# Optimization experiments

Measured on AMD Instinct MI355X. Metric: run time of the kernel, lower is better.

## Reference

```python
import jax, jax.numpy as jnp
import numpy as np

B, T, S = 4, 1024, 1024
E, H, D, M = 768, 12, 64, 3072
SCALE = 1.0 / (D ** 0.5)
EPS = 1e-5


def setup_inputs() -> dict:
    key = jax.random.key(0)
    ks = jax.random.split(key, 20)
    s = 0.02

    def n(k, shp):
        return jax.random.normal(k, shp, jnp.float32) * s

    return {
        "target": jax.random.normal(ks[0], (B, T, E), jnp.float32),
        "memory": jax.random.normal(ks[1], (B, S, E), jnp.float32),
        # self-attention: per-head Q/K/V projections stacked over heads [H,E,D]
        "sa_wq": n(ks[2], (H, E, D)), "sa_bq": jnp.zeros((H, D), jnp.float32),
        "sa_wk": n(ks[3], (H, E, D)), "sa_bk": jnp.zeros((H, D), jnp.float32),
        "sa_wv": n(ks[4], (H, E, D)), "sa_bv": jnp.zeros((H, D), jnp.float32),
        "sa_wo": n(ks[5], (H * D, E)), "sa_bo": jnp.zeros((E,), jnp.float32),
        # cross-attention
        "ca_wq": n(ks[6], (H, E, D)), "ca_bq": jnp.zeros((H, D), jnp.float32),
        "ca_wk": n(ks[7], (H, E, D)), "ca_bk": jnp.zeros((H, D), jnp.float32),
        "ca_wv": n(ks[8], (H, E, D)), "ca_bv": jnp.zeros((H, D), jnp.float32),
        "ca_wo": n(ks[9], (H * D, E)), "ca_bo": jnp.zeros((E,), jnp.float32),
        # layernorms
        "ln1_g": jnp.ones((E,), jnp.float32), "ln1_b": jnp.zeros((E,), jnp.float32),
        "ln2_g": jnp.ones((E,), jnp.float32), "ln2_b": jnp.zeros((E,), jnp.float32),
        "ln3_g": jnp.ones((E,), jnp.float32), "ln3_b": jnp.zeros((E,), jnp.float32),
        # FFN
        "ffn_w1": n(ks[10], (E, M)), "ffn_b1": jnp.zeros((M,), jnp.float32),
        "ffn_w2": n(ks[11], (M, E)), "ffn_b2": jnp.zeros((E,), jnp.float32),
    }


def layernorm(x, g, b):
    mu = jnp.mean(x, axis=-1, keepdims=True)
    var = jnp.mean(jnp.square(x - mu), axis=-1, keepdims=True)
    return (x - mu) * jax.lax.rsqrt(var + EPS) * g + b


def mha(q_in, k_in, v_in, wq, bq, wk, bk, wv, bv, wo, bo, mask=None):
    # batched equivalent of the per-head looped projections
    Q = jnp.einsum('bse,hed->bhsd', q_in, wq) + bq[None, :, None, :]
    K = jnp.einsum('bte,hed->bhtd', k_in, wk) + bk[None, :, None, :]
    V = jnp.einsum('bte,hed->bhtd', v_in, wv) + bv[None, :, None, :]
    scores = jnp.einsum('bhsd,bhtd->bhst', Q, K) * SCALE
    if mask is not None:
        scores = jnp.where(mask, scores, -jnp.inf)
    w = jax.nn.softmax(scores, axis=-1)
    o = jnp.einsum('bhst,bhtd->bhsd', w, V)  # [B,H,Sq,D]
    o = o.transpose(0, 2, 1, 3).reshape(q_in.shape[0], q_in.shape[1], H * D)
    return o @ wo + bo


def reference(target, memory,
              sa_wq, sa_bq, sa_wk, sa_bk, sa_wv, sa_bv, sa_wo, sa_bo,
              ca_wq, ca_bq, ca_wk, ca_bk, ca_wv, ca_bv, ca_wo, ca_bo,
              ln1_g, ln1_b, ln2_g, ln2_b, ln3_g, ln3_b,
              ffn_w1, ffn_b1, ffn_w2, ffn_b2):
    Tq = target.shape[1]
    causal = jnp.tril(jnp.ones((Tq, Tq), bool))  # [T,T], broadcasts over B,H
    # pre-norm self-attention + residual
    x = layernorm(target, ln1_g, ln1_b)
    x = mha(x, x, x, sa_wq, sa_bq, sa_wk, sa_bk, sa_wv, sa_bv, sa_wo, sa_bo, causal) + target
    # pre-norm cross-attention + residual
    res = x
    y = layernorm(x, ln2_g, ln2_b)
    x = mha(y, memory, memory, ca_wq, ca_bq, ca_wk, ca_bk, ca_wv, ca_bv, ca_wo, ca_bo) + res
    # pre-norm FFN (Linear -> GELU -> Linear) + residual
    res = x
    y = layernorm(x, ln3_g, ln3_b)
    x = jax.nn.gelu(y @ ffn_w1 + ffn_b1) @ ffn_w2 + ffn_b2 + res
    return x
```

## Files before the change

kernel.cpp:

```cpp
#include <hip/hip_runtime.h>
#include <hip/hip_bf16.h>
#include <stdint.h>

#define BB 4
#define TT 1024
#define SS 1024
#define EE 768
#define HH 12
#define DDIM 64
#define MM 3072
#define NROWS 4096
#define SCALE2 0.18033688011112042f

typedef unsigned short u16;
using short8 = __attribute__((ext_vector_type(8))) short;
using f32x4  = __attribute__((ext_vector_type(4))) float;

__device__ inline f32x4 mfma16(short8 a, short8 b, f32x4 c) {
  return __builtin_amdgcn_mfma_f32_16x16x32_bf16(a, b, c, 0, 0, 0);
}

__device__ inline float b2f(u16 u) {
  union { uint32_t i; float f; } z; z.i = ((uint32_t)u) << 16; return z.f;
}
__device__ inline u16 f2b(float f) {
  __hip_bfloat16 h = __float2bfloat16(f);
  return *reinterpret_cast<u16*>(&h);
}
__device__ inline float loadf(const float* p) { return *p; }
__device__ inline float loadf(const u16* p) { return b2f(*p); }

__device__ inline float tanh_f(float x) {
  float e = exp2f(x * 2.885390081777927f);
  return 1.0f - 2.0f / (e + 1.0f);
}
__device__ inline float gelu_f(float x) {
  const float k0 = 0.7978845608028654f;
  const float k1 = 0.044715f;
  float t = tanh_f(k0 * (x + k1 * x * x * x));
  return 0.5f * x * (1.0f + t);
}

__device__ inline void gload16(const u16* g, u16* l) {
  __builtin_amdgcn_global_load_lds(
      (const __attribute__((address_space(1))) unsigned int*)g,
      (__attribute__((address_space(3))) unsigned int*)l, 16, 0, 0);
}

__global__ __launch_bounds__(256) void prep_k(
    const float* __restrict__ target, const float* __restrict__ ln1_g,
    const float* __restrict__ ln1_b, u16* __restrict__ lnb,
    const float* __restrict__ mem, u16* __restrict__ memB,
    const float* __restrict__ bq3, const float* __restrict__ bk3,
    const float* __restrict__ bv3, float* __restrict__ d3,
    const float* __restrict__ bk2, const float* __restrict__ bv2,
    float* __restrict__ d2,
    const float* __restrict__ sa_wq, const float* __restrict__ sa_wk,
    const float* __restrict__ sa_wv, u16* __restrict__ wqkvT_sa,
    const float* __restrict__ ca_wq, const float* __restrict__ ca_wk,
    const float* __restrict__ ca_wv, u16* __restrict__ wqkvT_ca,
    const float* __restrict__ sa_wo, const float* __restrict__ ca_wo,
    u16* __restrict__ woT,
    const float* __restrict__ ffn_w1, u16* __restrict__ w1T,
    const float* __restrict__ ffn_w2, u16* __restrict__ w2T) {
  __shared__ u16 tile[32][34];
  __shared__ float red[8];
  const int blk = blockIdx.x, t = threadIdx.x;
  if (blk < 4096) {
    const float* xr = target + (size_t)blk * EE;
    float v0 = xr[t], v1 = xr[t + 256], v2 = xr[t + 512];
    float s = v0 + v1 + v2;
#pragma unroll
    for (int m = 32; m >= 1; m >>= 1) s += __shfl_xor(s, m);
    int wv = t >> 6, ln = t & 63;
    if (ln == 0) red[wv] = s;
    __syncthreads();
    float mean = (red[0] + red[1] + red[2] + red[3]) * (1.0f / EE);
    float e0 = v0 - mean, e1 = v1 - mean, e2 = v2 - mean;
    float s2 = e0 * e0 + e1 * e1 + e2 * e2;
#pragma unroll
    for (int m = 32; m >= 1; m >>= 1) s2 += __shfl_xor(s2, m);
    if (ln == 0) red[4 + wv] = s2;
    __syncthreads();
    float var = (red[4] + red[5] + red[6] + red[7]) * (1.0f / EE);
    float rstd = rsqrtf(var + 1e-5f);
    u16* yr = lnb + (size_t)blk * EE;
    yr[t]       = f2b(e0 * rstd * ln1_g[t]       + ln1_b[t]);
    yr[t + 256] = f2b(e1 * rstd * ln1_g[t + 256] + ln1_b[t + 256]);
    yr[t + 512] = f2b(e2 * rstd * ln1_g[t + 512] + ln1_b[t + 512]);
  } else if (blk < 7168) {
    int i = ((blk - 4096) * 256 + t) * 4;
    float4 f = *(const float4*)(mem + i);
    u16 o[4] = {f2b(f.x), f2b(f.y), f2b(f.z), f2b(f.w)};
    *(uint64_t*)(memB + i) = *(const uint64_t*)o;
  } else if (blk < 7177) {
    int i = (blk - 7168) * 256 + t;
    if (i < 768) d3[i] = bq3[i];
    else if (i < 1536) d3[i] = bk3[i - 768];
    else d3[i] = bv3[i - 1536];
  } else if (blk < 7183) {
    int i = (blk - 7177) * 256 + t;
    if (i < 768) d2[i] = bk2[i];
    else d2[i] = bv2[i - 768];
  } else {
    const float* ip; u16* op; int R, C, bx, by;
    int r = blk - 7183;
    if (r < 1728) {
      int u = r / 48, rr = r % 48; bx = rr & 1; by = rr >> 1;
      const float* s = (u < 12) ? sa_wq : (u < 24) ? sa_wk : sa_wv;
      ip = s + (size_t)(u % 12) * EE * DDIM;
      op = wqkvT_sa + (size_t)u * EE * DDIM;
      R = EE; C = DDIM;
    } else if (r < 3456) {
      r -= 1728;
      int u = r / 48, rr = r % 48; bx = rr & 1; by = rr >> 1;
      const float* s = (u < 12) ? ca_wq : (u < 24) ? ca_wk : ca_wv;
      ip = s + (size_t)(u % 12) * EE * DDIM;
      op = wqkvT_ca + (size_t)u * EE * DDIM;
      R = EE; C = DDIM;
    } else if (r < 4608) {
      r -= 3456;
      int u = r / 576, rr = r % 576; bx = rr % 24; by = rr / 24;
      ip = (u == 0) ? sa_wo : ca_wo;
      op = woT + (size_t)u * EE * EE;
      R = EE; C = EE;
    } else if (r < 6912) {
      r -= 4608; bx = r % 96; by = r / 96;
      ip = ffn_w1; op = w1T; R = EE; C = MM;
    } else {
      r -= 6912; bx = r % 24; by = r / 24;
      ip = ffn_w2; op = w2T; R = MM; C = EE;
    }
    int r0 = by * 32, c0 = bx * 32;
    int tx = t & 31, ty = t >> 5;
#pragma unroll
    for (int j = 0; j < 32; j += 8)
      tile[ty + j][tx] = f2b(ip[(size_t)(r0 + ty + j) * C + (c0 + tx)]);
    __syncthreads();
#pragma unroll
    for (int j = 0; j < 32; j += 8)
      op[(size_t)(c0 + ty + j) * R + (r0 + tx)] = tile[tx][ty + j];
  }
}

template <typename T>
__global__ __launch_bounds__(256) void layernorm_k(const T* __restrict__ x,
    const float* __restrict__ g, const float* __restrict__ b,
    u16* __restrict__ y) {
  int row = blockIdx.x, t = threadIdx.x;
  const T* xr = x + (size_t)row * EE;
  float v0 = loadf(xr + t), v1 = loadf(xr + t + 256), v2 = loadf(xr + t + 512);
  float s = v0 + v1 + v2;
#pragma unroll
  for (int m = 32; m >= 1; m >>= 1) s += __shfl_xor(s, m);
  __shared__ float red[8];
  int wv = t >> 6, ln = t & 63;
  if (ln == 0) red[wv] = s;
  __syncthreads();
  float mean = (red[0] + red[1] + red[2] + red[3]) * (1.0f / EE);
  float d0 = v0 - mean, d1 = v1 - mean, d2 = v2 - mean;
  float s2 = d0 * d0 + d1 * d1 + d2 * d2;
#pragma unroll
  for (int m = 32; m >= 1; m >>= 1) s2 += __shfl_xor(s2, m);
  if (ln == 0) red[4 + wv] = s2;
  __syncthreads();
  float var = (red[4] + red[5] + red[6] + red[7]) * (1.0f / EE);
  float rstd = rsqrtf(var + 1e-5f);
  u16* yr = y + (size_t)row * EE;
  yr[t]       = f2b(d0 * rstd * g[t]       + b[t]);
  yr[t + 256] = f2b(d1 * rstd * g[t + 256] + b[t + 256]);
  yr[t + 512] = f2b(d2 * rstd * g[t + 512] + b[t + 512]);
}

template <int RESMODE, bool GELU, int XCDSWZ, typename OutT>
__global__ __launch_bounds__(256) void gemm128_k(
    const u16* __restrict__ A, const u16* __restrict__ Bt,
    const float* __restrict__ bias, const void* __restrict__ res,
    OutT* __restrict__ C, int M, int N, int K) {
  __shared__ u16 As[2][128 * 32];
  __shared__ u16 Bs[2][128 * 32];
  int bx = blockIdx.x, by = blockIdx.y;
  if (XCDSWZ == 1) {
    const int nbx = N >> 7;
    int id = bx + nbx * by;
    int per = (nbx * (M >> 7)) >> 3;
    int sid = (id & 7) * per + (id >> 3);
    bx = sid % nbx; by = sid / nbx;
  } else if (XCDSWZ == 2) {
    const int nbx = N >> 7, hx = nbx >> 1, qy = (M >> 7) >> 2;
    int id = bx + nbx * by;
    int xcd = id & 7, j = id >> 3;
    int rx = xcd & 1, ry = xcd >> 1;
    bx = rx * hx + j % hx;
    by = ry * qy + j / hx;
  }
  const int bm = by * 128, bn = bx * 128;
  const int t = threadIdx.x;
  const int wave = t >> 6, lane = t & 63;
  const int wr = wave >> 1, wc = wave & 1;
  const int g = lane >> 4, li = lane & 15;
  f32x4 acc[4][4] = {};
  const size_t rowskip = (size_t)64 * K;
  const int scol = (((t & 3) ^ ((t >> 3) & 3)) * 8);
  const u16* Ag = A + (size_t)(bm + (t >> 2)) * K + scol;
  const u16* Bg = Bt + (size_t)(bn + (t >> 2)) * K + scol;

  gload16(Ag, &As[0][t * 8]);
  gload16(Ag + rowskip, &As[0][2048 + t * 8]);
  gload16(Bg, &Bs[0][t * 8]);
  gload16(Bg + rowskip, &Bs[0][2048 + t * 8]);
  __syncthreads();

  const int nsteps = K >> 5;
#define STEP128(CUR, NXT, SB)                                                  \
  {                                                                            \
    if ((SB) + 1 < nsteps) {                                                   \
      const int k0 = ((SB) + 1) << 5;                                          \
      gload16(Ag + k0, &As[NXT][t * 8]);                                       \
      gload16(Ag + rowskip + k0, &As[NXT][2048 + t * 8]);                      \
      gload16(Bg + k0, &Bs[NXT][t * 8]);                                       \
      gload16(Bg + rowskip + k0, &Bs[NXT][2048 + t * 8]);                      \
    }                                                                          \
    short8 af[4], bf[4];                                                       \
    _Pragma("unroll")                                                          \
    for (int i = 0; i < 4; i++) {                                              \
      const int ar = wr * 64 + i * 16 + li;                                    \
      af[i] = *(const short8*)(&As[CUR][ar * 32 + ((g ^ ((ar >> 1) & 3)) * 8)]); \
      const int br = wc * 64 + i * 16 + li;                                    \
      bf[i] = *(const short8*)(&Bs[CUR][br * 32 + ((g ^ ((br >> 1) & 3)) * 8)]); \
    }                                                                          \
    _Pragma("unroll")                                                          \
    for (int mi = 0; mi < 4; mi++)                                             \
      _Pragma("unroll")                                                        \
      for (int nj = 0; nj < 4; nj++)                                           \
        acc[mi][nj] = mfma16(af[mi], bf[nj], acc[mi][nj]);                     \
    __syncthreads();                                                           \
  }
  for (int s = 0; s < nsteps; s += 2) {
    STEP128(0, 1, s)
    STEP128(1, 0, s + 1)
  }
#undef STEP128

#pragma unroll
  for (int mi = 0; mi < 4; mi++)
#pragma unroll
    for (int nj = 0; nj < 4; nj++) {
      int n = bn + wc * 64 + nj * 16 + li;
      float bv = bias[n];
#pragma unroll
      for (int i = 0; i < 4; i++) {
        int m = bm + wr * 64 + mi * 16 + g * 4 + i;
        float val = acc[mi][nj][i] + bv;
        if (GELU) val = gelu_f(val);
        if (RESMODE == 1) val += ((const float*)res)[(size_t)m * N + n];
        else if (RESMODE == 2) val += b2f(((const u16*)res)[(size_t)m * N + n]);
        if constexpr (sizeof(OutT) == 2) C[(size_t)m * N + n] = f2b(val);
        else                             C[(size_t)m * N + n] = val;
      }
    }
}

__global__ __launch_bounds__(256) void gemm128_dual_k(
    const u16* __restrict__ A0, const u16* __restrict__ B0,
    const float* __restrict__ bias0, u16* __restrict__ C0, int N0, int nbx0,
    const u16* __restrict__ A1, const u16* __restrict__ B1,
    const float* __restrict__ bias1, u16* __restrict__ C1, int N1,
    u16* __restrict__ vtsa, u16* __restrict__ vtca,
    int M, int K) {
  __shared__ u16 As[2][128 * 64];
  __shared__ u16 Bs[2][128 * 64];
  const int id = blockIdx.x + 30 * blockIdx.y;
  const int xcd = id & 7, j = id >> 3;
  const int rx = xcd & 1, ry = xcd >> 1;
  int x, y;
  if (j < 72) { x = rx * 9 + j % 9;               y = ry * 8 + j / 9; }
  else        { int jj = j - 72; x = 18 + rx * 6 + jj % 6; y = ry * 8 + jj / 6; }
  const bool p1 = (x >= nbx0);
  const u16* A = p1 ? A1 : A0;
  const u16* Bt = p1 ? B1 : B0;
  const float* bias = p1 ? bias1 : bias0;
  u16* C = p1 ? C1 : C0;
  const int N = p1 ? N1 : N0;
  const int bn = (p1 ? x - nbx0 : x) * 128;
  const int bm = y * 128;
  const int t = threadIdx.x;
  const int wave = t >> 6, lane = t & 63;
  const int wr = wave >> 1, wc = wave & 1;
  const int g = lane >> 4, li = lane & 15;
  f32x4 acc[4][4] = {};
  const int srow = t >> 3;
  const int scolz = ((t & 7) * 8) ^ ((srow & 7) << 3);
  const size_t skip32 = (size_t)32 * K;
  const u16* Ag = A + (size_t)(bm + srow) * K + scolz;
  const u16* Bg = Bt + (size_t)(bn + srow) * K + scolz;

#pragma unroll
  for (int jj = 0; jj < 4; jj++) {
    gload16(Ag + jj * skip32, &As[0][jj * 2048 + t * 8]);
    gload16(Bg + jj * skip32, &Bs[0][jj * 2048 + t * 8]);
  }
  __syncthreads();

  const int nsteps = K >> 6;
#define STEPD(CUR, NXT, SB)                                                    \
  {                                                                            \
    if ((SB) + 1 < nsteps) {                                                   \
      const int k0 = ((SB) + 1) << 6;                                          \
      _Pragma("unroll")                                                        \
      for (int jj = 0; jj < 4; jj++) {                                         \
        gload16(Ag + jj * skip32 + k0, &As[NXT][jj * 2048 + t * 8]);           \
        gload16(Bg + jj * skip32 + k0, &Bs[NXT][jj * 2048 + t * 8]);           \
      }                                                                        \
    }                                                                          \
    _Pragma("unroll")                                                          \
    for (int kk = 0; kk < 2; kk++) {                                           \
      short8 af[4], bf[4];                                                     \
      _Pragma("unroll")                                                        \
      for (int i = 0; i < 4; i++) {                                            \
        const int ar = wr * 64 + i * 16 + li;                                  \
        af[i] = *(const short8*)(&As[CUR][ar * 64 + ((kk * 32 + g * 8) ^ ((ar & 7) << 3))]); \
        const int br = wc * 64 + i * 16 + li;                                  \
        bf[i] = *(const short8*)(&Bs[CUR][br * 64 + ((kk * 32 + g * 8) ^ ((br & 7) << 3))]); \
      }                                                                        \
      _Pragma("unroll")                                                        \
      for (int mi = 0; mi < 4; mi++)                                           \
        _Pragma("unroll")                                                      \
        for (int nj = 0; nj < 4; nj++)                                         \
          acc[mi][nj] = mfma16(af[mi], bf[nj], acc[mi][nj]);                   \
    }                                                                          \
    __syncthreads();                                                           \
  }
  for (int s = 0; s < nsteps; s += 2) {
    STEPD(0, 1, s)
    STEPD(1, 0, s + 1)
  }
#undef STEPD

  const int vbase = p1 ? 768 : 1536;
  if (bn < vbase) {
#pragma unroll
    for (int mi = 0; mi < 4; mi++)
#pragma unroll
      for (int nj = 0; nj < 4; nj++) {
        int n = bn + wc * 64 + nj * 16 + li;
        float bv = bias[n];
#pragma unroll
        for (int i = 0; i < 4; i++) {
          int m = bm + wr * 64 + mi * 16 + g * 4 + i;
          C[(size_t)m * N + n] = f2b(acc[mi][nj][i] + bv);
        }
      }
  } else {
    u16* vtX = p1 ? vtca : vtsa;
    u16* tl = &As[0][0];
    const int bb = bm >> 10;
    const int t0b = bm & 1023;
#pragma unroll
    for (int nj = 0; nj < 4; nj++) {
      __syncthreads();
      {
        int n = bn + wc * 64 + nj * 16 + li;
        float bv = bias[n];
#pragma unroll
        for (int mi = 0; mi < 4; mi++)
#pragma unroll
          for (int i = 0; i < 4; i++) {
            int ml = wr * 64 + mi * 16 + g * 4 + i;
            tl[(wc * 16 + li) * 132 + ml] = f2b(acc[mi][nj][i] + bv);
          }
      }
      __syncthreads();
      int lr = t >> 3, m0 = (t & 7) * 16;
      int n = bn + (lr >> 4) * 64 + nj * 16 + (lr & 15);
      int hd = n - vbase;
      uint4 v0 = *(uint4*)&tl[lr * 132 + m0];
      uint4 v1 = *(uint4*)&tl[lr * 132 + m0 + 8];
      u16* dst = vtX + (((size_t)(bb * HH + (hd >> 6))) << 16) +
                 ((size_t)(hd & 63) << 10) + t0b + m0;
      *(uint4*)dst = v0;
      *(uint4*)(dst + 8) = v1;
    }
  }
}

template <int RESMODE, bool GELU, bool XCDSWZ, typename OutT>
__global__ __launch_bounds__(256) void gemm64_k(
    const u16* __restrict__ A, const u16* __restrict__ Bt,
    const float* __restrict__ bias, const void* __restrict__ res,
    OutT* __restrict__ C, int M, int N, int K) {
  __shared__ u16 As[2][64 * 64];
  __shared__ u16 Bs[2][64 * 64];
  int bx = blockIdx.x, by = blockIdx.y;
  if (XCDSWZ) {
    const int nbx = N >> 6;
    int id = bx + nbx * by;
    int per = (nbx * (M >> 6)) >> 3;
    int sid = (id & 7) * per + (id >> 3);
    bx = sid % nbx; by = sid / nbx;
  }
  const int bm = by * 64, bn = bx * 64;
  const int t = threadIdx.x;
  const int wave = t >> 6, lane = t & 63;
  const int wr = wave >> 1, wc = wave & 1;
  const int g = lane >> 4, li = lane & 15;
  f32x4 acc[2][2] = {};
  const int srow = t >> 3;
  const int scolz = ((t & 7) * 8) ^ ((srow & 7) << 3);
  const size_t skip32 = (size_t)32 * K;
  const u16* Ag = A + (size_t)(bm + srow) * K + scolz;
  const u16* Bg = Bt + (size_t)(bn + srow) * K + scolz;

  gload16(Ag, &As[0][t * 8]);
  gload16(Ag + skip32, &As[0][2048 + t * 8]);
  gload16(Bg, &Bs[0][t * 8]);
  gload16(Bg + skip32, &Bs[0][2048 + t * 8]);
  __syncthreads();

  const int nsteps = K >> 6;
#define STEP64(CUR, NXT, SB)                                                   \
  {                                                                            \
    if ((SB) + 1 < nsteps) {                                                   \
      const int k0 = ((SB) + 1) << 6;                                          \
      gload16(Ag + k0, &As[NXT][t * 8]);                                       \
      gload16(Ag + skip32 + k0, &As[NXT][2048 + t * 8]);                       \
      gload16(Bg + k0, &Bs[NXT][t * 8]);                                       \
      gload16(Bg + skip32 + k0, &Bs[NXT][2048 + t * 8]);                       \
    }                                                                          \
    short8 af[2][2], bf[2][2];                                                 \
    _Pragma("unroll")                                                          \
    for (int mt = 0; mt < 2; mt++)                                             \
      _Pragma("unroll")                                                        \
      for (int kk = 0; kk < 2; kk++) {                                         \
        int ar = wr * 32 + mt * 16 + li;                                       \
        af[mt][kk] = *(const short8*)(&As[CUR][ar * 64 + ((kk * 32 + g * 8) ^ ((ar & 7) << 3))]); \
        int br = wc * 32 + mt * 16 + li;                                       \
        bf[mt][kk] = *(const short8*)(&Bs[CUR][br * 64 + ((kk * 32 + g * 8) ^ ((br & 7) << 3))]); \
      }                                                                        \
    _Pragma("unroll")                                                          \
    for (int mt = 0; mt < 2; mt++)                                             \
      _Pragma("unroll")                                                        \
      for (int nt = 0; nt < 2; nt++)                                           \
        _Pragma("unroll")                                                      \
        for (int kk = 0; kk < 2; kk++)                                         \
          acc[mt][nt] = mfma16(af[mt][kk], bf[nt][kk], acc[mt][nt]);           \
    __syncthreads();                                                           \
  }
  for (int s = 0; s < nsteps; s += 2) {
    STEP64(0, 1, s)
    STEP64(1, 0, s + 1)
  }
#undef STEP64

#pragma unroll
  for (int mt = 0; mt < 2; mt++)
#pragma unroll
    for (int nt = 0; nt < 2; nt++) {
      int n = bn + wc * 32 + nt * 16 + li;
      float bv = bias[n];
#pragma unroll
      for (int i = 0; i < 4; i++) {
        int m = bm + wr * 32 + mt * 16 + g * 4 + i;
        float val = acc[mt][nt][i] + bv;
        if (GELU) val = gelu_f(val);
        if (RESMODE == 1) val += ((const float*)res)[(size_t)m * N + n];
        else if (RESMODE == 2) val += b2f(((const u16*)res)[(size_t)m * N + n]);
        if constexpr (sizeof(OutT) == 2) C[(size_t)m * N + n] = f2b(val);
        else                             C[(size_t)m * N + n] = val;
      }
    }
}

template <bool CAUSAL>
__global__ __launch_bounds__(256) void attn4_k(
    const u16* __restrict__ Q, const u16* __restrict__ K,
    const u16* __restrict__ VT, u16* __restrict__ O,
    int ldq, int ldk) {
  int b, h, q0;
  if (CAUSAL) {
    int id = blockIdx.x;
    int cu = id & 255, slot = id >> 8;
    int q, hb;
    if (cu < 96) {
      int p = cu & 1, r = cu >> 1;
      q = (slot == 0 ? 0 : slot == 1 ? 6 : 14) + p;
      hb = r;
    } else if (cu < 192) {
      int c2 = cu - 96; int p = c2 & 1, r = c2 >> 1;
      q = (slot == 0 ? 2 : slot == 1 ? 8 : 12) + p;
      hb = r;
    } else if (cu < 224) {
      int c2 = cu - 192;
      int p = c2 & 1, r = c2 >> 1;
      if (slot == 0)      { q = 10;    hb = c2; }
      else if (slot == 1) { q = 11;    hb = c2; }
      else                { q = 4 + p; hb = r; }
    } else {
      int c2 = cu - 224;
      int p = c2 & 1, r = c2 >> 1;
      if (slot == 0)      { q = 4;      hb = 16 + c2; }
      else if (slot == 1) { q = 5;      hb = 16 + c2; }
      else                { q = 10 + p; hb = 32 + r; }
    }
    h = hb % HH; b = hb / HH; q0 = q * 64;
  } else {
    int id = blockIdx.x + 16 * (blockIdx.y + HH * (int)blockIdx.z);
    int sid = (id & 7) * 96 + (id >> 3);
    q0 = (sid & 15) * 64;
    int yz = sid >> 4;
    h = yz % HH; b = yz / HH;
  }
  int tid = threadIdx.x, wave = tid >> 6, lane = tid & 63;
  int g = lane >> 4, li = lane & 15;
  const u16* Qb = Q + (size_t)b * TT * ldq + h * DDIM;
  const u16* Kb = K + (size_t)b * SS * ldk + h * DDIM;
  const u16* Vb = VT + (size_t)(b * HH + h) * DDIM * SS;
  u16* Ob = O + (size_t)b * TT * EE + h * DDIM;

  __shared__ u16 Ks[128 * 64];
  __shared__ u16 Vs[64 * 128];
  u16* Psw = &Ks[wave * 2048];

  int qrow = q0 + wave * 16 + li;
  short8 qf0 = *(const short8*)(Qb + (size_t)qrow * ldq + g * 8);
  short8 qf1 = *(const short8*)(Qb + (size_t)qrow * ldq + 32 + g * 8);

  f32x4 accO[4] = {};
  float lrow[4] = {0.f, 0.f, 0.f, 0.f};

  const int krow = tid >> 3;
  const int vrow = tid >> 4;
  const int qmax = q0 + wave * 16 + 15;

  int kvEnd = CAUSAL ? (((q0 + 64 + 127) >> 7) << 7) : SS;
  for (int kv0 = 0; kv0 < kvEnd; kv0 += 128) {
#pragma unroll
    for (int j = 0; j < 4; j++) {
      int kr = j * 32 + krow;
      int kc = ((tid & 7) * 8) ^ ((kr & 7) << 3);
      gload16(Kb + (size_t)(kv0 + kr) * ldk + kc, &Ks[j * 2048 + tid * 8]);
    }
#pragma unroll
    for (int j = 0; j < 4; j++) {
      int vr = j * 16 + vrow;
      int vc = ((tid & 15) * 8) ^ ((vr & 15) << 3);
      gload16(Vb + (size_t)vr * SS + kv0 + vc, &Vs[j * 2048 + tid * 8]);
    }
    __syncthreads();

    {
      const bool needMask = CAUSAL && (kv0 + 127 > qmax);
      f32x4 s[8];
#pragma unroll
      for (int kt = 0; kt < 8; kt++) {
        int kr = kt * 16 + li;
        int sw = (kr & 7) << 3;
        short8 kf0 = *(const short8*)(&Ks[kr * 64 + ((g * 8) ^ sw)]);
        short8 kf1 = *(const short8*)(&Ks[kr * 64 + ((g * 8 + 32) ^ sw)]);
        f32x4 z = {};
        z = mfma16(qf0, kf0, z);
        z = mfma16(qf1, kf1, z);
        s[kt] = z;
      }
      __syncthreads();

      float rsum[4] = {0.f, 0.f, 0.f, 0.f};
#pragma unroll
      for (int kt = 0; kt < 8; kt++)
#pragma unroll
        for (int i = 0; i < 4; i++) {
          float sv = s[kt][i] * SCALE2;
          if (needMask) {
            int qi = q0 + wave * 16 + g * 4 + i;
            int ti = kv0 + kt * 16 + li;
            if (ti > qi) sv = -1e30f;
          }
          float p = exp2f(sv);
          s[kt][i] = p;
          rsum[i] += p;
        }
#pragma unroll
      for (int msk = 1; msk < 16; msk <<= 1)
#pragma unroll
        for (int i = 0; i < 4; i++) rsum[i] += __shfl_xor(rsum[i], msk);
#pragma unroll
      for (int i = 0; i < 4; i++) lrow[i] += rsum[i];

#pragma unroll
      for (int kt = 0; kt < 8; kt++)
#pragma unroll
        for (int i = 0; i < 4; i++) {
          int row = g * 4 + i;
          Psw[row * 128 + ((kt * 16 + li) ^ ((row & 15) << 3))] = f2b(s[kt][i]);
        }

#pragma unroll
      for (int tc = 0; tc < 4; tc++) {
        short8 pf = *(const short8*)(&Psw[li * 128 + ((tc * 32 + g * 8) ^ ((li & 15) << 3))]);
#pragma unroll
        for (int dt = 0; dt < 4; dt++) {
          int vr = dt * 16 + li;
          short8 vf = *(const short8*)(&Vs[vr * 128 + ((tc * 32 + g * 8) ^ ((vr & 15) << 3))]);
          accO[dt] = mfma16(pf, vf, accO[dt]);
        }
      }
    }
    __syncthreads();
  }

#pragma unroll
  for (int i = 0; i < 4; i++) {
    float inv = 1.0f / lrow[i];
    int q = q0 + wave * 16 + g * 4 + i;
#pragma unroll
    for (int dt = 0; dt < 4; dt++)
      Ob[(size_t)q * EE + dt * 16 + li] = f2b(accO[dt][i] * inv);
  }
}

static inline void* wsoff(void* ws, size_t& off, size_t bytes) {
  void* p = (char*)ws + off;
  off += (bytes + 255) & ~(size_t)255;
  return p;
}

extern "C" void kernel_launch(void* const* d_in, const int* in_sizes, int n_in,
                              void* d_out, int out_size, void* d_ws, size_t ws_size,
                              hipStream_t stream) {
  const float* target = (const float*)d_in[0];
  const float* memory = (const float*)d_in[1];
  const float* sa_wq = (const float*)d_in[2];  const float* sa_bq = (const float*)d_in[3];
  const float* sa_wk = (const float*)d_in[4];  const float* sa_bk = (const float*)d_in[5];
  const float* sa_wv = (const float*)d_in[6];  const float* sa_bv = (const float*)d_in[7];
  const float* sa_wo = (const float*)d_in[8];  const float* sa_bo = (const float*)d_in[9];
  const float* ca_wq = (const float*)d_in[10]; const float* ca_bq = (const float*)d_in[11];
  const float* ca_wk = (const float*)d_in[12]; const float* ca_bk = (const float*)d_in[13];
  const float* ca_wv = (const float*)d_in[14]; const float* ca_bv = (const float*)d_in[15];
  const float* ca_wo = (const float*)d_in[16]; const float* ca_bo = (const float*)d_in[17];
  const float* ln1_g = (const float*)d_in[18]; const float* ln1_b = (const float*)d_in[19];
  const float* ln2_g = (const float*)d_in[20]; const float* ln2_b = (const float*)d_in[21];
  const float* ln3_g = (const float*)d_in[22]; const float* ln3_b = (const float*)d_in[23];
  const float* ffn_w1 = (const float*)d_in[24]; const float* ffn_b1 = (const float*)d_in[25];
  const float* ffn_w2 = (const float*)d_in[26]; const float* ffn_b2 = (const float*)d_in[27];

  size_t off = 0;
  const size_t WB = (size_t)EE * EE * 2;
  u16* wqkvT_sa = (u16*)wsoff(d_ws, off, 3 * WB);
  u16* wqT_ca   = (u16*)wsoff(d_ws, off, WB);
  u16* wkvT_ca  = (u16*)wsoff(d_ws, off, 2 * WB);
  u16* woT_sa   = (u16*)wsoff(d_ws, off, WB);
  u16* woT_ca   = (u16*)wsoff(d_ws, off, WB);
  u16* w1T      = (u16*)wsoff(d_ws, off, (size_t)EE * MM * 2);
  u16* w2T      = (u16*)wsoff(d_ws, off, (size_t)EE * MM * 2);
  float* bsa_qkv = (float*)wsoff(d_ws, off, 2304 * 4);
  float* bca_kv  = (float*)wsoff(d_ws, off, 1536 * 4);
  const size_t AB = (size_t)NROWS * EE * 2;
  u16* mx2   = (u16*)wsoff(d_ws, off, AB);
  u16* lnb   = (u16*)wsoff(d_ws, off, AB);
  u16* S2    = (u16*)wsoff(d_ws, off, 3 * AB);
  u16* S3    = (u16*)wsoff(d_ws, off, AB);
  u16* x1    = (u16*)wsoff(d_ws, off, AB);
  u16* vtsa  = (u16*)wsoff(d_ws, off, AB);
  u16* vtca  = (u16*)wsoff(d_ws, off, AB);
  u16* kvca  = (u16*)wsoff(d_ws, off, 2 * AB);
  u16* qkv_sa = S2;
  u16* qb_ca  = S2;
  u16* attn_out = S3;
  u16* f1     = S2;
  u16* memB   = mx2;
  u16* x2     = mx2;

  prep_k<<<16399, 256, 0, stream>>>(
      target, ln1_g, ln1_b, lnb,
      memory, memB,
      sa_bq, sa_bk, sa_bv, bsa_qkv, ca_bk, ca_bv, bca_kv,
      sa_wq, sa_wk, sa_wv, wqkvT_sa,
      ca_wq, ca_wk, ca_wv, wqT_ca,
      sa_wo, ca_wo, woT_sa,
      ffn_w1, w1T, ffn_w2, w2T);

  gemm128_dual_k<<<dim3(30, 32), 256, 0, stream>>>(
      lnb, wqkvT_sa, bsa_qkv, qkv_sa, 3 * EE, 18,
      memB, wkvT_ca, bca_kv, kvca, 2 * EE,
      vtsa, vtca, NROWS, EE);

  attn4_k<true><<<dim3(768, 1, 1), 256, 0, stream>>>(
      qkv_sa, qkv_sa + EE, vtsa, attn_out, 3 * EE, 3 * EE);
  gemm64_k<1, false, true, u16><<<dim3(12, 64), 256, 0, stream>>>(
      attn_out, woT_sa, sa_bo, target, x1, NROWS, EE, EE);

  layernorm_k<u16><<<NROWS, 256, 0, stream>>>(x1, ln2_g, ln2_b, lnb);
  gemm64_k<0, false, true, u16><<<dim3(12, 64), 256, 0, stream>>>(
      lnb, wqT_ca, ca_bq, nullptr, qb_ca, NROWS, EE, EE);
  attn4_k<false><<<dim3(16, 12, 4), 256, 0, stream>>>(
      qb_ca, kvca, vtca, attn_out, EE, 2 * EE);
  gemm64_k<2, false, true, u16><<<dim3(12, 64), 256, 0, stream>>>(
      attn_out, woT_ca, ca_bo, x1, x2, NROWS, EE, EE);

  layernorm_k<u16><<<NROWS, 256, 0, stream>>>(x2, ln3_g, ln3_b, lnb);
  gemm128_k<0, true, 2, u16><<<dim3(24, 32), 256, 0, stream>>>(
      lnb, w1T, ffn_b1, nullptr, f1, NROWS, MM, EE);
  gemm64_k<2, false, true, float><<<dim3(12, 64), 256, 0, stream>>>(
      f1, w2T, ffn_b2, x2, (float*)d_out, NROWS, EE, MM);
}
```

Measured before the change: 222.7 us.

## Double-buffer K/V tiles in attention kernel to overlap loads with compute

```diff
diff --git a/kernel.cpp b/kernel.cpp
--- a/kernel.cpp
+++ b/kernel.cpp
@@ -517,9 +517,8 @@
   const u16* Vb = VT + (size_t)(b * HH + h) * DDIM * SS;
   u16* Ob = O + (size_t)b * TT * EE + h * DDIM;
 
-  __shared__ u16 Ks[128 * 64];
-  __shared__ u16 Vs[64 * 128];
-  u16* Psw = &Ks[wave * 2048];
+  __shared__ u16 Ks[2][128 * 64];
+  __shared__ u16 Vs[2][64 * 128];
 
   int qrow = q0 + wave * 16 + li;
   short8 qf0 = *(const short8*)(Qb + (size_t)qrow * ldq + g * 8);
@@ -529,84 +528,106 @@
   float lrow[4] = {0.f, 0.f, 0.f, 0.f};
 
   const int krow = tid >> 3;
+  const int kcb  = (tid & 7) * 8;
   const int vrow = tid >> 4;
+  const int vcb  = (tid & 15) * 8;
   const int qmax = q0 + wave * 16 + 15;
 
-  int kvEnd = CAUSAL ? (((q0 + 64 + 127) >> 7) << 7) : SS;
-  for (int kv0 = 0; kv0 < kvEnd; kv0 += 128) {
-#pragma unroll
-    for (int j = 0; j < 4; j++) {
-      int kr = j * 32 + krow;
-      int kc = ((tid & 7) * 8) ^ ((kr & 7) << 3);
-      gload16(Kb + (size_t)(kv0 + kr) * ldk + kc, &Ks[j * 2048 + tid * 8]);
-    }
-#pragma unroll
-    for (int j = 0; j < 4; j++) {
-      int vr = j * 16 + vrow;
-      int vc = ((tid & 15) * 8) ^ ((vr & 15) << 3);
-      gload16(Vb + (size_t)vr * SS + kv0 + vc, &Vs[j * 2048 + tid * 8]);
-    }
-    __syncthreads();
-
-    {
-      const bool needMask = CAUSAL && (kv0 + 127 > qmax);
-      f32x4 s[8];
-#pragma unroll
-      for (int kt = 0; kt < 8; kt++) {
-        int kr = kt * 16 + li;
-        int sw = (kr & 7) << 3;
-        short8 kf0 = *(const short8*)(&Ks[kr * 64 + ((g * 8) ^ sw)]);
-        short8 kf1 = *(const short8*)(&Ks[kr * 64 + ((g * 8 + 32) ^ sw)]);
-        f32x4 z = {};
-        z = mfma16(qf0, kf0, z);
-        z = mfma16(qf1, kf1, z);
-        s[kt] = z;
-      }
-      __syncthreads();
-
-      float rsum[4] = {0.f, 0.f, 0.f, 0.f};
-#pragma unroll
-      for (int kt = 0; kt < 8; kt++)
-#pragma unroll
-        for (int i = 0; i < 4; i++) {
-          float sv = s[kt][i] * SCALE2;
-          if (needMask) {
-            int qi = q0 + wave * 16 + g * 4 + i;
-            int ti = kv0 + kt * 16 + li;
-            if (ti > qi) sv = -1e30f;
-          }
-          float p = exp2f(sv);
-          s[kt][i] = p;
-          rsum[i] += p;
-        }
-#pragma unroll
-      for (int msk = 1; msk < 16; msk <<= 1)
-#pragma unroll
-        for (int i = 0; i < 4; i++) rsum[i] += __shfl_xor(rsum[i], msk);
-#pragma unroll
-      for (int i = 0; i < 4; i++) lrow[i] += rsum[i];
-
-#pragma unroll
-      for (int kt = 0; kt < 8; kt++)
-#pragma unroll
-        for (int i = 0; i < 4; i++) {
-          int row = g * 4 + i;
-          Psw[row * 128 + ((kt * 16 + li) ^ ((row & 15) << 3))] = f2b(s[kt][i]);
-        }
-
-#pragma unroll
-      for (int tc = 0; tc < 4; tc++) {
-        short8 pf = *(const short8*)(&Psw[li * 128 + ((tc * 32 + g * 8) ^ ((li & 15) << 3))]);
-#pragma unroll
-        for (int dt = 0; dt < 4; dt++) {
-          int vr = dt * 16 + li;
-          short8 vf = *(const short8*)(&Vs[vr * 128 + ((tc * 32 + g * 8) ^ ((vr & 15) << 3))]);
-          accO[dt] = mfma16(pf, vf, accO[dt]);
-        }
-      }
-    }
-    __syncthreads();
-  }
+  const int nt = CAUSAL ? ((q0 + 191) >> 7) : (SS >> 7);
+
+#define STAGE_K(BUF, T1) {                                                     \
+    const int kv = (T1) << 7;                                                  \
+    _Pragma("unroll")                                                          \
+    for (int j = 0; j < 4; j++) {                                              \
+      int kr = j * 32 + krow;                                                  \
+      int kc = kcb ^ ((kr & 7) << 3);                                          \
+      gload16(Kb + (size_t)(kv + kr) * ldk + kc, &Ks[BUF][j * 2048 + tid * 8]); \
+    }                                                                          \
+  }
+#define STAGE_V(BUF, T1) {                                                     \
+    const int kv = (T1) << 7;                                                  \
+    _Pragma("unroll")                                                          \
+    for (int j = 0; j < 4; j++) {                                              \
+      int vr = j * 16 + vrow;                                                  \
+      int vc = vcb ^ ((vr & 15) << 3);                                         \
+      gload16(Vb + (size_t)vr * SS + kv + vc, &Vs[BUF][j * 2048 + tid * 8]);   \
+    }                                                                          \
+  }
+
+#define ATTNSTEP(CUR, NXT, T, PREF) {                                          \
+    if (PREF) STAGE_K(NXT, (T) + 1)                                            \
+    const int kv0 = (T) << 7;                                                  \
+    const bool needMask = CAUSAL && (kv0 + 127 > qmax);                        \
+    f32x4 s[8];                                                                \
+    _Pragma("unroll")                                                          \
+    for (int kt = 0; kt < 8; kt++) {                                           \
+      int kr = kt * 16 + li;                                                   \
+      int sw = (kr & 7) << 3;                                                  \
+      short8 kf0 = *(const short8*)(&Ks[CUR][kr * 64 + ((g * 8) ^ sw)]);       \
+      short8 kf1 = *(const short8*)(&Ks[CUR][kr * 64 + ((g * 8 + 32) ^ sw)]);  \
+      f32x4 z = {};                                                            \
+      z = mfma16(qf0, kf0, z);                                                 \
+      z = mfma16(qf1, kf1, z);                                                 \
+      s[kt] = z;                                                               \
+    }                                                                          \
+    __syncthreads();               \
+    if (PREF) STAGE_V(NXT, (T) + 1)                                            \
+    float rsum[4] = {0.f, 0.f, 0.f, 0.f};                                      \
+    _Pragma("unroll")                                                          \
+    for (int kt = 0; kt < 8; kt++)                                             \
+      _Pragma("unroll")                                                        \
+      for (int i = 0; i < 4; i++) {                                            \
+        float sv = s[kt][i] * SCALE2;                                          \
+        if (needMask) {                                                        \
+          int qi = q0 + wave * 16 + g * 4 + i;                                 \
+          int ti = kv0 + kt * 16 + li;                                         \
+          if (ti > qi) sv = -1e30f;                                            \
+        }                                                                      \
+        float p = exp2f(sv);                                                   \
+        s[kt][i] = p;                                                          \
+        rsum[i] += p;                                                          \
+      }                                                                        \
+    _Pragma("unroll")                                                          \
+    for (int msk = 1; msk < 16; msk <<= 1)                                     \
+      _Pragma("unroll")                                                        \
+      for (int i = 0; i < 4; i++) rsum[i] += __shfl_xor(rsum[i], msk);         \
+    _Pragma("unroll")                                                          \
+    for (int i = 0; i < 4; i++) lrow[i] += rsum[i];                            \
+    u16* Psw = &Ks[CUR][wave * 2048];                                          \
+    _Pragma("unroll")                                                          \
+    for (int kt = 0; kt < 8; kt++)                                             \
+      _Pragma("unroll")                                                        \
+      for (int i = 0; i < 4; i++) {                                            \
+        int row = g * 4 + i;                                                   \
+        Psw[row * 128 + ((kt * 16 + li) ^ ((row & 15) << 3))] = f2b(s[kt][i]); \
+      }                                                                        \
+    _Pragma("unroll")                                                          \
+    for (int tc = 0; tc < 4; tc++) {                                           \
+      short8 pf = *(const short8*)(&Psw[li * 128 + ((tc * 32 + g * 8) ^ ((li & 15) << 3))]); \
+      _Pragma("unroll")                                                        \
+      for (int dt = 0; dt < 4; dt++) {                                         \
+        int vr = dt * 16 + li;                                                 \
+        short8 vf = *(const short8*)(&Vs[CUR][vr * 128 + ((tc * 32 + g * 8) ^ ((vr & 15) << 3))]); \
+        accO[dt] = mfma16(pf, vf, accO[dt]);                                   \
+      }                                                                        \
+    }                                                                          \
+    __syncthreads();                \
+  }
+
+  STAGE_K(0, 0)
+  STAGE_V(0, 0)
+  __syncthreads();
+
+  int t2 = 0;
+  for (; t2 + 1 < nt; t2 += 2) {
+    ATTNSTEP(0, 1, t2, true)
+    ATTNSTEP(1, 0, t2 + 1, (t2 + 2) < nt)
+  }
+  if (t2 < nt) ATTNSTEP(0, 1, t2, false)
+
+#undef ATTNSTEP
+#undef STAGE_K
+#undef STAGE_V
 
 #pragma unroll
   for (int i = 0; i < 4; i++) {
```

Result: slower. 229.0 us (+2.9%).
